# Optimization experiments

Hardware: AMD Instinct MI355X
Metric: run time of the kernel (lower is better)

The kernel has to match this reference:

```python
import jax, jax.numpy as jnp
import numpy as np

B, C, D, H, EXP = 4, 1024, 1024, 16, 4
EPS = 1e-6


def ffn_layernorm(x, w, b):
    # normalize over channel axis (dim 1); w,b have shape (1, C)
    u = jnp.mean(x, axis=1, keepdims=True)
    s = jnp.mean((x - u) ** 2, axis=1, keepdims=True)
    xn = (x - u) / jnp.sqrt(s + EPS)
    return w[:, :, None] * xn + b[:, :, None]


def softmax_one(x):
    # exp(x - max) / (1 + sum exp(x - max)), exactly as the torch SoftmaxOne
    m = jnp.max(x, axis=-1, keepdims=True)
    e = jnp.exp(x - m)
    return e / (1.0 + jnp.sum(e, axis=-1, keepdims=True))


def setup_inputs() -> dict:
    key = jax.random.key(0)
    ks = jax.random.split(key, 20)
    n = lambda k, shape, s=0.02: jax.random.normal(k, shape, dtype=jnp.float32) * s
    inp = {
        "x1": jax.random.normal(ks[0], (B, C, D), dtype=jnp.float32),
        "lnq_w": jnp.ones((1, C), jnp.float32) + n(ks[1], (1, C)),
        "lnq_b": n(ks[2], (1, C)),
        "lnk_w": jnp.ones((1, C), jnp.float32) + n(ks[3], (1, C)),
        "lnk_b": n(ks[4], (1, C)),
        "lnv_w": jnp.ones((1, C), jnp.float32) + n(ks[5], (1, C)),
        "lnv_b": n(ks[6], (1, C)),
        "wq": n(ks[7], (D, D)),
        "bq": n(ks[8], (D,)),
        "wk": n(ks[9], (D, D)),
        "bk": n(ks[10], (D,)),
        "wv": n(ks[11], (D, D)),
        "bv": n(ks[12], (D,)),
        "ffnln_w": jnp.ones((1, C), jnp.float32) + n(ks[13], (1, C)),
        "ffnln_b": n(ks[14], (1, C)),
        "conv1_w": n(ks[15], (C * EXP, C)),
        "conv1_b": n(ks[16], (C * EXP,)),
        "conv2_w": n(ks[17], (C, C * EXP)),
        "conv2_b": n(ks[18], (C,)),
    }
    return inp


def reference(x1, lnq_w, lnq_b, lnk_w, lnk_b, lnv_w, lnv_b,
              wq, bq, wk, bk, wv, bv,
              ffnln_w, ffnln_b, conv1_w, conv1_b, conv2_w, conv2_b):
    b, c, d = x1.shape
    dh = d // H
    q = ffn_layernorm(x1, lnq_w, lnq_b)
    k = ffn_layernorm(x1, lnk_w, lnk_b)
    v = ffn_layernorm(x1, lnv_w, lnv_b)
    # nn.Linear: y = x @ W.T + b, then the torch code's direct reshape
    # (b, c, d) -> (b, H, c, dh) (NOT a transpose-split)
    q = (q @ wq.T + bq).reshape(b, H, c, dh)
    k = (k @ wk.T + bk).reshape(b, H, c, dh)
    v = (v @ wv.T + bv).reshape(b, H, c, dh)
    scale = 1.0 / np.sqrt(dh).astype(np.float32)
    attn = jnp.einsum("bhqe,bhke->bhqk", q * scale, k)
    attn_weights = softmax_one(attn)
    o = jnp.einsum("bhqk,bhke->bhqe", attn_weights, v)
    o = o.transpose(0, 2, 1, 3).reshape(b, c, d)
    x = x1 + o
    # FFN: channel LayerNorm -> 1x1 conv (channel mix) -> GELU -> 1x1 conv
    xl = ffn_layernorm(x, ffnln_w, ffnln_b)
    h1 = jnp.einsum("oc,bcl->bol", conv1_w, xl) + conv1_b[None, :, None]
    h1 = jax.nn.gelu(h1, approximate=False)
    h2 = jnp.einsum("oc,bcl->bol", conv2_w, h1) + conv2_b[None, :, None]
    return (x + h2, attn_weights)
```

## Files before the change

### kernel.cpp

```cpp
#include <hip/hip_runtime.h>
#include <hip/hip_bf16.h>
#include <math.h>


typedef __bf16 bf16;
typedef __bf16 bf16x4 __attribute__((ext_vector_type(4)));
typedef __bf16 bf16x8 __attribute__((ext_vector_type(8)));
typedef float floatx4 __attribute__((ext_vector_type(4)));

#define MFMA16(a, b, c) __builtin_amdgcn_mfma_f32_16x16x32_bf16(a, b, c, 0, 0, 0)

__device__ __forceinline__ void gload16(const void* g, void* l) {
    __builtin_amdgcn_global_load_lds((__attribute__((address_space(1))) void*)g,
                                     (__attribute__((address_space(3))) void*)l,
                                     16, 0, 0);
}

__global__ __launch_bounds__(256)
void cast_all(const float* __restrict__ s0, bf16* __restrict__ d0_,
              const float* __restrict__ s1, bf16* __restrict__ d1_,
              const float* __restrict__ s2, bf16* __restrict__ d2_,
              const float* __restrict__ s3, bf16* __restrict__ d3_,
              const float* __restrict__ s4, bf16* __restrict__ d4_)
{
    int blk = blockIdx.x;
    const float* s; bf16* d; int base;
    if (blk < 1024)      { s = s0; d = d0_; base = blk; }
    else if (blk < 2048) { s = s1; d = d1_; base = blk - 1024; }
    else if (blk < 3072) { s = s2; d = d2_; base = blk - 2048; }
    else if (blk < 7168) { s = s3; d = d3_; base = blk - 3072; }
    else                 { s = s4; d = d4_; base = blk - 7168; }
    long i = ((long)base << 10) + (threadIdx.x << 2);
    float4 v = *(const float4*)(s + i);
    bf16x4 o;
    o[0] = (bf16)v.x; o[1] = (bf16)v.y; o[2] = (bf16)v.z; o[3] = (bf16)v.w;
    *(bf16x4*)(d + i) = o;
}

__global__ __launch_bounds__(256)
void stats_part(const float* __restrict__ xin, float* __restrict__ ps,
                float* __restrict__ pq)
{
    __shared__ float S1[4][64];
    __shared__ float S2[4][64];
    const int b = blockIdx.z, chunk = blockIdx.y;
    const int d0 = blockIdx.x << 6;
    const int tid = threadIdx.x;
    const int dl = tid & 63, cg = tid >> 6;
    const float* xp = xin + ((long)b << 20) + d0 + dl;
    const int cbase = (chunk << 8) + (cg << 6);
    float s = 0.f, sq = 0.f;
    for (int c = 0; c < 64; ++c) {
        float v = xp[(long)(cbase + c) << 10];
        s += v; sq += v * v;
    }
    S1[cg][dl] = s; S2[cg][dl] = sq;
    __syncthreads();
    if (tid < 64) {
        float ts = S1[0][tid] + S1[1][tid] + S1[2][tid] + S1[3][tid];
        float tq = S2[0][tid] + S2[1][tid] + S2[2][tid] + S2[3][tid];
        int idx = ((b * 4 + chunk) << 10) + d0 + tid;
        ps[idx] = ts; pq[idx] = tq;
    }
}

__global__ __launch_bounds__(256)
void stats_fin(const float* __restrict__ ps, const float* __restrict__ pq,
               float* __restrict__ u, float* __restrict__ rstd)
{
    int i = (blockIdx.x << 8) + threadIdx.x;
    int b = i >> 10, d = i & 1023;
    int base = (b << 12) + d;
    float s = ps[base] + ps[base + 1024] + ps[base + 2048] + ps[base + 3072];
    float q = pq[base] + pq[base + 1024] + pq[base + 2048] + pq[base + 3072];
    float mu = s * (1.f / 1024.f);
    float var = q * (1.f / 1024.f) - mu * mu;
    u[i] = mu;
    rstd[i] = rsqrtf(var + 1e-6f);
}

__global__ __launch_bounds__(256)
void ln_qkv_kernel(const float* __restrict__ x1, const float* __restrict__ u,
                   const float* __restrict__ rs,
                   const float* __restrict__ wq, const float* __restrict__ bq,
                   const float* __restrict__ wk, const float* __restrict__ bk,
                   const float* __restrict__ wv, const float* __restrict__ bv,
                   bf16* __restrict__ lnq, bf16* __restrict__ lnk,
                   bf16* __restrict__ lnv)
{
    const int bc = blockIdx.x;
    const int c = bc & 1023, b = bc >> 10;
    const int d = threadIdx.x << 2;
    const long i = ((long)bc << 10) + d;
    const float4 xv = *(const float4*)(x1 + i);
    const float4 uv = *(const float4*)(u + (b << 10) + d);
    const float4 rv = *(const float4*)(rs + (b << 10) + d);
    float xn0 = (xv.x - uv.x) * rv.x;
    float xn1 = (xv.y - uv.y) * rv.y;
    float xn2 = (xv.z - uv.z) * rv.z;
    float xn3 = (xv.w - uv.w) * rv.w;
    float sw, sb; bf16x4 o;
    sw = wq[c]; sb = bq[c];
    o[0]=(bf16)(sw*xn0+sb); o[1]=(bf16)(sw*xn1+sb); o[2]=(bf16)(sw*xn2+sb); o[3]=(bf16)(sw*xn3+sb);
    *(bf16x4*)(lnq + i) = o;
    sw = wk[c]; sb = bk[c];
    o[0]=(bf16)(sw*xn0+sb); o[1]=(bf16)(sw*xn1+sb); o[2]=(bf16)(sw*xn2+sb); o[3]=(bf16)(sw*xn3+sb);
    *(bf16x4*)(lnk + i) = o;
    sw = wv[c]; sb = bv[c];
    o[0]=(bf16)(sw*xn0+sb); o[1]=(bf16)(sw*xn1+sb); o[2]=(bf16)(sw*xn2+sb); o[3]=(bf16)(sw*xn3+sb);
    *(bf16x4*)(lnv + i) = o;
}

__global__ __launch_bounds__(256)
void gemm_bt(const bf16* __restrict__ Ab, const bf16* __restrict__ Bb,
             void* __restrict__ Outb, float* __restrict__ Part,
             const float* __restrict__ bias0, const float* __restrict__ bias1,
             const float* __restrict__ bias2, const float* __restrict__ residb,
             long sAz, long sBz, long sOz, long sRz, long sPz,
             int M, int N, int K, int Ksub, int zdiv, int mode)
{
    __shared__ __align__(16) bf16 As[128 * 32];
    __shared__ __align__(16) bf16 Bs[128 * 32];
    const int z = blockIdx.z;
    const int zb = z / zdiv, kz = z % zdiv;
    const bf16* A = Ab + (long)zb * sAz + (long)kz * Ksub;
    const bf16* B = Bb + (long)zb * sBz + (long)kz * Ksub;
    const float* bias = (zb == 0) ? bias0 : (zb == 1 ? bias1 : bias2);
    const int m0 = blockIdx.y << 7, n0 = blockIdx.x << 7;
    const int tid = threadIdx.x;
    const int wave = tid >> 6, lane = tid & 63;
    const int wm = (wave & 1) << 6, wn = (wave >> 1) << 6;
    const int lm = lane & 15, lk = (lane >> 4) << 3;
    floatx4 acc[4][4] = {};
    for (int kt = 0; kt < Ksub; kt += 32) {
        const bf16* Ag = A + (long)m0 * K + kt;
        const bf16* Bg = B + (long)n0 * K + kt;
#pragma unroll
        for (int i = 0; i < 2; ++i) {
            int c = tid + (i << 8);
            int row = c >> 2, kc = (c & 3) << 3;
            gload16(Ag + (long)row * K + kc, As + c * 8);
            gload16(Bg + (long)row * K + kc, Bs + c * 8);
        }
        __syncthreads();
        bf16x8 af[4], bfv[4];
#pragma unroll
        for (int mi = 0; mi < 4; ++mi)
            af[mi] = *(const bf16x8*)(As + (wm + mi * 16 + lm) * 32 + lk);
#pragma unroll
        for (int ni = 0; ni < 4; ++ni)
            bfv[ni] = *(const bf16x8*)(Bs + (wn + ni * 16 + lm) * 32 + lk);
#pragma unroll
        for (int mi = 0; mi < 4; ++mi)
#pragma unroll
            for (int ni = 0; ni < 4; ++ni)
                acc[mi][ni] = MFMA16(af[mi], bfv[ni], acc[mi][ni]);
        __syncthreads();
    }
    const int quad = lane >> 4;
    if (mode == 2) {
        if (kz == 0) {
            float* Out = (float*)Outb + (long)zb * sOz;
            const float* R = residb + (long)zb * sRz;
#pragma unroll
            for (int mi = 0; mi < 4; ++mi)
#pragma unroll
                for (int ni = 0; ni < 4; ++ni)
#pragma unroll
                    for (int r = 0; r < 4; ++r) {
                        int row = m0 + wm + mi * 16 + quad * 4 + r;
                        int col = n0 + wn + ni * 16 + lm;
                        long idx = (long)row * N + col;
                        Out[idx] = acc[mi][ni][r] + bias[row] + R[idx];
                    }
        } else {
            float* Out = Part + (long)zb * sPz;
#pragma unroll
            for (int mi = 0; mi < 4; ++mi)
#pragma unroll
                for (int ni = 0; ni < 4; ++ni)
#pragma unroll
                    for (int r = 0; r < 4; ++r) {
                        int row = m0 + wm + mi * 16 + quad * 4 + r;
                        int col = n0 + wn + ni * 16 + lm;
                        Out[(long)row * N + col] = acc[mi][ni][r];
                    }
        }
    } else {
        bf16* Out = (bf16*)Outb + (long)zb * sOz;
#pragma unroll
        for (int mi = 0; mi < 4; ++mi)
#pragma unroll
            for (int ni = 0; ni < 4; ++ni)
#pragma unroll
                for (int r = 0; r < 4; ++r) {
                    int row = m0 + wm + mi * 16 + quad * 4 + r;
                    int col = n0 + wn + ni * 16 + lm;
                    float v = acc[mi][ni][r] + bias[col];
                    if (mode == 1)
                        v = 0.5f * v * (1.0f + erff(v * 0.70710678118654752f));
                    Out[(long)row * N + col] = (bf16)v;
                }
    }
}

__global__ __launch_bounds__(256)
void addpart(float* __restrict__ out, const float* __restrict__ part)
{
    long i = (((long)blockIdx.x << 8) + threadIdx.x) << 2;
    float4 o = *(const float4*)(out + i);
    float4 p = *(const float4*)(part + i);
    o.x += p.x; o.y += p.y; o.z += p.z; o.w += p.w;
    *(float4*)(out + i) = o;
}

__global__ __launch_bounds__(256)
void vtrans_kernel(const bf16* __restrict__ v, bf16* __restrict__ vt)
{
    __shared__ bf16 T[64][66];
    const int p = blockIdx.y;
    const int k0 = blockIdx.x << 6;
    const bf16* V = v + ((long)p << 16);
    bf16* Vt = vt + ((long)p << 16);
    const int tid = threadIdx.x;
    const int e = tid & 63, g = tid >> 6;
#pragma unroll
    for (int j = 0; j < 16; ++j) {
        int kk = (g << 4) + j;
        T[e][kk] = V[((long)(k0 + kk) << 6) + e];
    }
    __syncthreads();
#pragma unroll
    for (int j = 0; j < 16; ++j) {
        int er = (g << 4) + j;
        Vt[((long)er << 10) + k0 + e] = T[er][e];
    }
}

__global__ __launch_bounds__(256)
void attn_kernel(const bf16* __restrict__ q, const bf16* __restrict__ k,
                 const bf16* __restrict__ vt, const float* __restrict__ x1,
                 float* __restrict__ attw, float* __restrict__ x)
{
    __shared__ __align__(16) bf16 Wl[16][1032];
    __shared__ float red[16][4];
    const int s = blockIdx.x;
    const int p = blockIdx.y;
    const int b = p >> 4, h = p & 15;
    const bf16* Qp = q + ((long)b << 20) + ((long)h << 16);
    const bf16* Kp = k + ((long)b << 20) + ((long)h << 16);
    const bf16* Vt = vt + ((long)p << 16);
    const int tid = threadIdx.x, w = tid >> 6, lane = tid & 63;
    const int lm = lane & 15, quad = lane >> 4;
    const int r0 = s << 4, kc0 = w << 8;

    floatx4 acc[16];
#pragma unroll
    for (int t = 0; t < 16; ++t) acc[t] = (floatx4){0.f, 0.f, 0.f, 0.f};

#pragma unroll
    for (int e0 = 0; e0 < 64; e0 += 32) {
        bf16x8 aq = *(const bf16x8*)(Qp + ((long)(r0 + lm) << 6) + e0 + quad * 8);
#pragma unroll
        for (int t = 0; t < 16; ++t) {
            bf16x8 bk = *(const bf16x8*)(Kp + ((long)(kc0 + t * 16 + lm) << 6) + e0 + quad * 8);
            acc[t] = MFMA16(aq, bk, acc[t]);
        }
    }
#pragma unroll
    for (int t = 0; t < 16; ++t)
#pragma unroll
        for (int r = 0; r < 4; ++r) acc[t][r] *= 0.125f;

    float mloc[4];
#pragma unroll
    for (int r = 0; r < 4; ++r) {
        float mm = acc[0][r];
#pragma unroll
        for (int t = 1; t < 16; ++t) mm = fmaxf(mm, acc[t][r]);
        mloc[r] = mm;
    }
#pragma unroll
    for (int off = 1; off < 16; off <<= 1)
#pragma unroll
        for (int r = 0; r < 4; ++r) mloc[r] = fmaxf(mloc[r], __shfl_xor(mloc[r], off, 64));
    if (lm == 0)
#pragma unroll
        for (int r = 0; r < 4; ++r) red[quad * 4 + r][w] = mloc[r];
    __syncthreads();
    float mfin[4];
#pragma unroll
    for (int r = 0; r < 4; ++r) {
        int row = quad * 4 + r;
        mfin[r] = fmaxf(fmaxf(red[row][0], red[row][1]), fmaxf(red[row][2], red[row][3]));
    }
    float sloc[4] = {0.f, 0.f, 0.f, 0.f};
#pragma unroll
    for (int t = 0; t < 16; ++t)
#pragma unroll
        for (int r = 0; r < 4; ++r) {
            float e = __expf(acc[t][r] - mfin[r]);
            acc[t][r] = e;
            sloc[r] += e;
        }
#pragma unroll
    for (int off = 1; off < 16; off <<= 1)
#pragma unroll
        for (int r = 0; r < 4; ++r) sloc[r] += __shfl_xor(sloc[r], off, 64);
    __syncthreads();
    if (lm == 0)
#pragma unroll
        for (int r = 0; r < 4; ++r) red[quad * 4 + r][w] = sloc[r];
    __syncthreads();
    float inv[4];
#pragma unroll
    for (int r = 0; r < 4; ++r) {
        int row = quad * 4 + r;
        inv[r] = 1.f / (1.f + red[row][0] + red[row][1] + red[row][2] + red[row][3]);
    }
#pragma unroll
    for (int r = 0; r < 4; ++r) {
        int row = quad * 4 + r;
        float iv = inv[r];
#pragma unroll
        for (int t = 0; t < 16; ++t)
            Wl[row][kc0 + t * 16 + lm] = (bf16)(acc[t][r] * iv);
    }
    __syncthreads();

    floatx4 opv[4];
#pragma unroll
    for (int ni = 0; ni < 4; ++ni) opv[ni] = (floatx4){0.f, 0.f, 0.f, 0.f};
#pragma unroll
    for (int i = 0; i < 8; ++i) {
        const int kk = kc0 + i * 32;
        bf16x8 a0 = *(const bf16x8*)&Wl[lm][kk + quad * 8];
#pragma unroll
        for (int ni = 0; ni < 4; ++ni) {
            bf16x8 bv = *(const bf16x8*)(Vt + ((long)(ni * 16 + lm) << 10) + kk + quad * 8);
            opv[ni] = MFMA16(a0, bv, opv[ni]);
        }
    }
    {
        float* attp = attw + ((long)p << 20) + ((long)r0 << 10);
#pragma unroll
        for (int i = 0; i < 16; ++i) {
            int v4 = (i << 8) + tid;
            int row = v4 >> 8, col = (v4 & 255) << 2;
            bf16x4 wv = *(const bf16x4*)&Wl[row][col];
            floatx4 o = {(float)wv[0], (float)wv[1], (float)wv[2], (float)wv[3]};
            __builtin_nontemporal_store(o, (floatx4*)(attp + ((long)row << 10) + col));
        }
    }
    __syncthreads();
    float* Ored = (float*)&Wl[0][0];
#pragma unroll
    for (int ni = 0; ni < 4; ++ni)
#pragma unroll
        for (int r = 0; r < 4; ++r)
            Ored[(w * 16 + quad * 4 + r) * 64 + ni * 16 + lm] = opv[ni][r];
    __syncthreads();
    const float* x1p = x1 + ((long)b << 20) + ((long)r0 << 10) + (h << 6);
    float* xp = x + ((long)b << 20) + ((long)r0 << 10) + (h << 6);
#pragma unroll
    for (int j = 0; j < 4; ++j) {
        int el = tid + (j << 8);
        int row = el >> 6, cc = el & 63;
        float o = Ored[row * 64 + cc] + Ored[(16 + row) * 64 + cc]
                + Ored[(32 + row) * 64 + cc] + Ored[(48 + row) * 64 + cc];
        xp[((long)row << 10) + cc] = x1p[((long)row << 10) + cc] + o;
    }
}

__global__ __launch_bounds__(256)
void ln_ffn_t_kernel(const float* __restrict__ x, const float* __restrict__ u2,
                     const float* __restrict__ r2, const float* __restrict__ fw,
                     const float* __restrict__ fb, bf16* __restrict__ xlT)
{
    __shared__ bf16 T[64][66];
    const int b = blockIdx.z;
    const int l0 = blockIdx.x << 6, c0 = blockIdx.y << 6;
    const int tid = threadIdx.x;
    const int ll = tid & 63, g = tid >> 6;
    const float uu = u2[(b << 10) + l0 + ll];
    const float rr = r2[(b << 10) + l0 + ll];
#pragma unroll
    for (int j = 0; j < 16; ++j) {
        int cc = (g << 4) + j;
        float v = x[((long)b << 20) + ((long)(c0 + cc) << 10) + l0 + ll];
        T[ll][cc] = (bf16)(fw[c0 + cc] * (v - uu) * rr + fb[c0 + cc]);
    }
    __syncthreads();
#pragma unroll
    for (int j = 0; j < 16; ++j) {
        int lr = (g << 4) + j;
        xlT[((long)b << 20) + ((long)(l0 + lr) << 10) + c0 + ll] = T[lr][ll];
    }
}

extern "C" void kernel_launch(void* const* d_in, const int* in_sizes, int n_in,
                              void* d_out, int out_size, void* d_ws, size_t ws_size,
                              hipStream_t stream)
{
    const float* x1      = (const float*)d_in[0];
    const float* lnq_w   = (const float*)d_in[1];
    const float* lnq_b   = (const float*)d_in[2];
    const float* lnk_w   = (const float*)d_in[3];
    const float* lnk_b   = (const float*)d_in[4];
    const float* lnv_w   = (const float*)d_in[5];
    const float* lnv_b   = (const float*)d_in[6];
    const float* wq      = (const float*)d_in[7];
    const float* bq      = (const float*)d_in[8];
    const float* wk      = (const float*)d_in[9];
    const float* bk      = (const float*)d_in[10];
    const float* wv      = (const float*)d_in[11];
    const float* bv      = (const float*)d_in[12];
    const float* ffnln_w = (const float*)d_in[13];
    const float* ffnln_b = (const float*)d_in[14];
    const float* conv1_w = (const float*)d_in[15];
    const float* conv1_b = (const float*)d_in[16];
    const float* conv2_w = (const float*)d_in[17];
    const float* conv2_b = (const float*)d_in[18];
    (void)in_sizes; (void)n_in; (void)out_size; (void)ws_size;

    char* ws = (char*)d_ws;
    const size_t OFF_VT   = 262144;
    const size_t OFF_QKV  = OFF_VT   + 8388608;
    const size_t OFF_WQKV = OFF_QKV  + 25165824;
    const size_t OFF_W1   = OFF_WQKV + 8388608;
    const size_t OFF_X    = OFF_W1   + 8388608;
    const size_t OFF_W2   = OFF_X    + 16777216;
    float* u1    = (float*)(ws + 0);
    float* r1    = (float*)(ws + 16384);
    float* u2    = (float*)(ws + 32768);
    float* r2    = (float*)(ws + 49152);
    float* ps    = (float*)(ws + 65536);
    float* pq    = (float*)(ws + 131072);
    bf16*  vt    = (bf16*)(ws + OFF_VT);
    bf16*  qkv   = (bf16*)(ws + OFF_QKV);
    bf16*  wqkvb = (bf16*)(ws + OFF_WQKV);
    bf16*  w1b   = (bf16*)(ws + OFF_W1);
    float* x     = (float*)(ws + OFF_X);
    bf16*  w2b   = (bf16*)(ws + OFF_W2);
    bf16*  h1T   = (bf16*)(ws + OFF_VT);
    bf16*  xlT   = (bf16*)(ws + OFF_WQKV);
    float* part  = (float*)(ws + OFF_WQKV);

    float* out0 = (float*)d_out;
    float* attw = (float*)((char*)d_out + 16777216);
    bf16*  lnqkv = (bf16*)attw;

    cast_all<<<11264, 256, 0, stream>>>(wq, wqkvb, wk, wqkvb + (1 << 20),
                                        wv, wqkvb + (2 << 20), conv1_w, w1b, conv2_w, w2b);
    stats_part<<<dim3(16, 4, 4), 256, 0, stream>>>(x1, ps, pq);
    stats_fin<<<16, 256, 0, stream>>>(ps, pq, u1, r1);
    ln_qkv_kernel<<<4096, 256, 0, stream>>>(x1, u1, r1, lnq_w, lnq_b, lnk_w, lnk_b,
                                            lnv_w, lnv_b, lnqkv, lnqkv + (1L << 22),
                                            lnqkv + (2L << 22));
    gemm_bt<<<dim3(8, 32, 3), 256, 0, stream>>>(lnqkv, wqkvb, qkv, nullptr, bq, bk, bv,
                                                nullptr, 1L << 22, 1L << 20, 1L << 22, 0, 0,
                                                4096, 1024, 1024, 1024, 1, 0);
    vtrans_kernel<<<dim3(16, 64), 256, 0, stream>>>(qkv + (2L << 22), vt);
    attn_kernel<<<dim3(64, 64), 256, 0, stream>>>(qkv, qkv + (1L << 22), vt, x1, attw, x);
    stats_part<<<dim3(16, 4, 4), 256, 0, stream>>>(x, ps, pq);
    stats_fin<<<16, 256, 0, stream>>>(ps, pq, u2, r2);
    ln_ffn_t_kernel<<<dim3(16, 16, 4), 256, 0, stream>>>(x, u2, r2, ffnln_w, ffnln_b, xlT);
    gemm_bt<<<dim3(32, 8, 4), 256, 0, stream>>>(xlT, w1b, h1T, nullptr, conv1_b, conv1_b,
                                                conv1_b, nullptr, 1L << 20, 0, 1L << 22, 0, 0,
                                                1024, 4096, 1024, 1024, 1, 1);
    gemm_bt<<<dim3(8, 8, 8), 256, 0, stream>>>(w2b, h1T, out0, part, conv2_b, conv2_b,
                                               conv2_b, x, 0, 1L << 22, 1L << 20, 1L << 20,
                                               1L << 20, 1024, 1024, 4096, 2048, 2, 2);
    addpart<<<4096, 256, 0, stream>>>(out0, part);
}
```

Before: 675.5 us.

## Double-buffer GEMM with 64-wide K tiles, XOR swizzle, and remap attention grid

The GEMM is rewritten as a templated kernel. It uses 64-wide K tiles held in double-buffered LDS, so global-to-LDS loads for the next tile overlap the MFMAs on the current one. An XOR swizzle is added to cut LDS bank conflicts, and setprio is raised around the MFMA block. Launch bounds now request 2 blocks per CU, and the mode is a compile-time template parameter. The attention kernel moves to a 1D grid whose index mapping interleaves (batch, head) pairs, aiming for better cache locality. LDS use rises to 64KB per block, which may limit occupancy.

```diff
diff --git a/kernel.cpp b/kernel.cpp
--- a/kernel.cpp
+++ b/kernel.cpp
@@ -111,16 +111,17 @@
     *(bf16x4*)(lnv + i) = o;
 }
 
-__global__ __launch_bounds__(256)
-void gemm_bt(const bf16* __restrict__ Ab, const bf16* __restrict__ Bb,
+template<int MODE>
+__global__ __launch_bounds__(256, 2)
+void gemm_nt(const bf16* __restrict__ Ab, const bf16* __restrict__ Bb,
              void* __restrict__ Outb, float* __restrict__ Part,
              const float* __restrict__ bias0, const float* __restrict__ bias1,
              const float* __restrict__ bias2, const float* __restrict__ residb,
              long sAz, long sBz, long sOz, long sRz, long sPz,
-             int M, int N, int K, int Ksub, int zdiv, int mode)
-{
-    __shared__ __align__(16) bf16 As[128 * 32];
-    __shared__ __align__(16) bf16 Bs[128 * 32];
+             int M, int N, int K, int Ksub, int zdiv)
+{
+    __shared__ __align__(16) bf16 As[2][128 * 64];
+    __shared__ __align__(16) bf16 Bs[2][128 * 64];
     const int z = blockIdx.z;
     const int zb = z / zdiv, kz = z % zdiv;
     const bf16* A = Ab + (long)zb * sAz + (long)kz * Ksub;
@@ -130,35 +131,63 @@
     const int tid = threadIdx.x;
     const int wave = tid >> 6, lane = tid & 63;
     const int wm = (wave & 1) << 6, wn = (wave >> 1) << 6;
-    const int lm = lane & 15, lk = (lane >> 4) << 3;
+    const int lm = lane & 15, quad = lane >> 4;
+    const int swz = (lm & 7) << 3;
+    const bf16* Ag = A + (long)m0 * K;
+    const bf16* Bg = B + (long)n0 * K;
+
     floatx4 acc[4][4] = {};
-    for (int kt = 0; kt < Ksub; kt += 32) {
-        const bf16* Ag = A + (long)m0 * K + kt;
-        const bf16* Bg = B + (long)n0 * K + kt;
-#pragma unroll
-        for (int i = 0; i < 2; ++i) {
-            int c = tid + (i << 8);
-            int row = c >> 2, kc = (c & 3) << 3;
-            gload16(Ag + (long)row * K + kc, As + c * 8);
-            gload16(Bg + (long)row * K + kc, Bs + c * 8);
-        }
+    const int nt = Ksub >> 6;
+
+#pragma unroll
+    for (int r_ = 0; r_ < 4; ++r_) {
+        int s_ = (r_ << 8) + tid;
+        int lrow = s_ >> 3;
+        long go = (long)lrow * K + (((s_ & 7) ^ (lrow & 7)) << 3);
+        gload16(Ag + go, &As[0][s_ << 3]);
+        gload16(Bg + go, &Bs[0][s_ << 3]);
+    }
+    __syncthreads();
+
+    for (int t = 0; t < nt; ++t) {
+        const int cur = t & 1;
+        if (t + 1 < nt) {
+            const int kofs = (t + 1) << 6;
+#pragma unroll
+            for (int r_ = 0; r_ < 4; ++r_) {
+                int s_ = (r_ << 8) + tid;
+                int lrow = s_ >> 3;
+                long go = (long)lrow * K + kofs + (((s_ & 7) ^ (lrow & 7)) << 3);
+                gload16(Ag + go, &As[cur ^ 1][s_ << 3]);
+                gload16(Bg + go, &Bs[cur ^ 1][s_ << 3]);
+            }
+        }
+        bf16x8 af[4][2], bfv[4][2];
+#pragma unroll
+        for (int i = 0; i < 4; ++i) {
+            int rA = (wm + i * 16 + lm) << 6;
+            int rB = (wn + i * 16 + lm) << 6;
+#pragma unroll
+            for (int ks = 0; ks < 2; ++ks) {
+                int co = (ks << 5) + (quad << 3);
+                af[i][ks]  = *(const bf16x8*)(&As[cur][(rA + co) ^ swz]);
+                bfv[i][ks] = *(const bf16x8*)(&Bs[cur][(rB + co) ^ swz]);
+            }
+        }
+        __builtin_amdgcn_s_setprio(1);
+#pragma unroll
+        for (int ks = 0; ks < 2; ++ks)
+#pragma unroll
+            for (int mi = 0; mi < 4; ++mi)
+#pragma unroll
+                for (int ni = 0; ni < 4; ++ni)
+                    acc[mi][ni] = MFMA16(af[mi][ks], bfv[ni][ks], acc[mi][ni]);
+        __builtin_amdgcn_s_setprio(0);
         __syncthreads();
-        bf16x8 af[4], bfv[4];
-#pragma unroll
-        for (int mi = 0; mi < 4; ++mi)
-            af[mi] = *(const bf16x8*)(As + (wm + mi * 16 + lm) * 32 + lk);
-#pragma unroll
-        for (int ni = 0; ni < 4; ++ni)
-            bfv[ni] = *(const bf16x8*)(Bs + (wn + ni * 16 + lm) * 32 + lk);
-#pragma unroll
-        for (int mi = 0; mi < 4; ++mi)
-#pragma unroll
-            for (int ni = 0; ni < 4; ++ni)
-                acc[mi][ni] = MFMA16(af[mi], bfv[ni], acc[mi][ni]);
-        __syncthreads();
-    }
-    const int quad = lane >> 4;
-    if (mode == 2) {
+    }
+
+    const int quad4 = quad << 2;
+    if (MODE == 2) {
         if (kz == 0) {
             float* Out = (float*)Outb + (long)zb * sOz;
             const float* R = residb + (long)zb * sRz;
@@ -168,7 +197,7 @@
                 for (int ni = 0; ni < 4; ++ni)
 #pragma unroll
                     for (int r = 0; r < 4; ++r) {
-                        int row = m0 + wm + mi * 16 + quad * 4 + r;
+                        int row = m0 + wm + mi * 16 + quad4 + r;
                         int col = n0 + wn + ni * 16 + lm;
                         long idx = (long)row * N + col;
                         Out[idx] = acc[mi][ni][r] + bias[row] + R[idx];
@@ -181,7 +210,7 @@
                 for (int ni = 0; ni < 4; ++ni)
 #pragma unroll
                     for (int r = 0; r < 4; ++r) {
-                        int row = m0 + wm + mi * 16 + quad * 4 + r;
+                        int row = m0 + wm + mi * 16 + quad4 + r;
                         int col = n0 + wn + ni * 16 + lm;
                         Out[(long)row * N + col] = acc[mi][ni][r];
                     }
@@ -194,10 +223,10 @@
             for (int ni = 0; ni < 4; ++ni)
 #pragma unroll
                 for (int r = 0; r < 4; ++r) {
-                    int row = m0 + wm + mi * 16 + quad * 4 + r;
+                    int row = m0 + wm + mi * 16 + quad4 + r;
                     int col = n0 + wn + ni * 16 + lm;
                     float v = acc[mi][ni][r] + bias[col];
-                    if (mode == 1)
+                    if (MODE == 1)
                         v = 0.5f * v * (1.0f + erff(v * 0.70710678118654752f));
                     Out[(long)row * N + col] = (bf16)v;
                 }
@@ -244,8 +273,9 @@
 {
     __shared__ __align__(16) bf16 Wl[16][1032];
     __shared__ float red[16][4];
-    const int s = blockIdx.x;
-    const int p = blockIdx.y;
+    const int bid = blockIdx.x;
+    const int p = ((bid & 7) << 3) | ((bid >> 3) & 7);
+    const int s = bid >> 6;
     const int b = p >> 4, h = p & 15;
     const bf16* Qp = q + ((long)b << 20) + ((long)h << 16);
     const bf16* Kp = k + ((long)b << 20) + ((long)h << 16);
@@ -457,19 +487,19 @@
     ln_qkv_kernel<<<4096, 256, 0, stream>>>(x1, u1, r1, lnq_w, lnq_b, lnk_w, lnk_b,
                                             lnv_w, lnv_b, lnqkv, lnqkv + (1L << 22),
                                             lnqkv + (2L << 22));
-    gemm_bt<<<dim3(8, 32, 3), 256, 0, stream>>>(lnqkv, wqkvb, qkv, nullptr, bq, bk, bv,
-                                                nullptr, 1L << 22, 1L << 20, 1L << 22, 0, 0,
-                                                4096, 1024, 1024, 1024, 1, 0);
+    gemm_nt<0><<<dim3(8, 32, 3), 256, 0, stream>>>(lnqkv, wqkvb, qkv, nullptr, bq, bk, bv,
+                                                   nullptr, 1L << 22, 1L << 20, 1L << 22, 0, 0,
+                                                   4096, 1024, 1024, 1024, 1);
     vtrans_kernel<<<dim3(16, 64), 256, 0, stream>>>(qkv + (2L << 22), vt);
-    attn_kernel<<<dim3(64, 64), 256, 0, stream>>>(qkv, qkv + (1L << 22), vt, x1, attw, x);
+    attn_kernel<<<4096, 256, 0, stream>>>(qkv, qkv + (1L << 22), vt, x1, attw, x);
     stats_part<<<dim3(16, 4, 4), 256, 0, stream>>>(x, ps, pq);
     stats_fin<<<16, 256, 0, stream>>>(ps, pq, u2, r2);
     ln_ffn_t_kernel<<<dim3(16, 16, 4), 256, 0, stream>>>(x, u2, r2, ffnln_w, ffnln_b, xlT);
-    gemm_bt<<<dim3(32, 8, 4), 256, 0, stream>>>(xlT, w1b, h1T, nullptr, conv1_b, conv1_b,
-                                                conv1_b, nullptr, 1L << 20, 0, 1L << 22, 0, 0,
-                                                1024, 4096, 1024, 1024, 1, 1);
-    gemm_bt<<<dim3(8, 8, 8), 256, 0, stream>>>(w2b, h1T, out0, part, conv2_b, conv2_b,
-                                               conv2_b, x, 0, 1L << 22, 1L << 20, 1L << 20,
-                                               1L << 20, 1024, 1024, 4096, 2048, 2, 2);
+    gemm_nt<1><<<dim3(32, 8, 4), 256, 0, stream>>>(xlT, w1b, h1T, nullptr, conv1_b, conv1_b,
+                                                   conv1_b, nullptr, 1L << 20, 0, 1L << 22, 0, 0,
+                                                   1024, 4096, 1024, 1024, 1);
+    gemm_nt<2><<<dim3(8, 8, 8), 256, 0, stream>>>(w2b, h1T, out0, part, conv2_b, conv2_b,
+                                                  conv2_b, x, 0, 1L << 22, 1L << 20, 1L << 20,
+                                                  1L << 20, 1024, 1024, 4096, 2048, 2);
     addpart<<<4096, 256, 0, stream>>>(out0, part);
 }
```

Result: faster. 624.9 us (-7.5%).
